# Kernel optimization log

Hardware: AMD Instinct MI355X
Metric: run time of the kernel (lower is better)

## Reference

```python
import jax, jax.numpy as jnp
import numpy as np

EMBED_DIM = 512
NUM_HEADS = 8
GLOBAL_MIX = 0.5


def setup_inputs() -> dict:
    key = jax.random.key(0)
    ks = jax.random.split(key, 7)
    B, L, E = 8, 1024, EMBED_DIM
    s = 1.0 / np.sqrt(E)
    x = jax.random.normal(ks[0], (B, L, E), dtype=jnp.float32)
    mask = jax.random.randint(ks[1], (B, L), 0, 2) > 0  # True = valid token
    Wq = jax.random.normal(ks[2], (E, E), dtype=jnp.float32) * s
    Wk = jax.random.normal(ks[3], (E, E), dtype=jnp.float32) * s
    Wv = jax.random.normal(ks[4], (E, E), dtype=jnp.float32) * s
    Wo = jax.random.normal(ks[5], (E, E), dtype=jnp.float32) * s
    G = jax.random.normal(ks[6], (L, L), dtype=jnp.float32)
    return {"x": x, "mask": mask, "Wq": Wq, "Wk": Wk, "Wv": Wv, "Wo": Wo, "G": G}


def _tanh_mha(x, mask, Wq, Wk, Wv, Wo, G):
    B, L, E = x.shape
    H = NUM_HEADS
    D = E // H
    scale = 1.0 / np.sqrt(D)
    dt = x.dtype
    fmax = jnp.finfo(dt).max
    tiny = jnp.finfo(dt).tiny

    def split_heads(t):  # (B,L,E) -> (B,H,L,D)
        return t.reshape(B, L, H, D).transpose(0, 2, 1, 3)

    q = split_heads(x @ Wq.T)
    k = split_heads(x @ Wk.T)
    v = split_heads(x @ Wv.T)

    scores = jnp.tanh(jnp.einsum('bhqd,bhkd->bhqk', q, k) * scale)
    key_valid = mask[:, None, None, :]  # (B,1,1,L)
    scores = jnp.where(key_valid, scores, -jnp.inf)

    finite = jnp.isfinite(scores)
    finite_scores = jnp.where(finite, scores, -fmax)
    m = jnp.max(finite_scores, axis=(1, 2, 3), keepdims=True)  # per-sample amax over heads+q+k
    m = jnp.where(jnp.isfinite(m), m, jnp.zeros_like(m))
    exp_scores = jnp.where(finite, jnp.exp(scores - m), jnp.zeros_like(scores))

    mf = mask.astype(dt)
    exp_scores = exp_scores * mf[:, None, None, :] * mf[:, None, :, None]
    denom = jnp.maximum(exp_scores.sum(axis=(1, 2, 3), keepdims=True), tiny)
    weights = exp_scores / denom
    # dropout p=0 -> identity; renorm pass kept for faithfulness
    renorm = jnp.maximum(weights.sum(axis=(1, 2, 3), keepdims=True), tiny)
    weights = weights / renorm

    # learnable global attention: softmax rows, clamp, mask, normalize over (q,k)
    activated = jnp.maximum(jax.nn.softmax(G, axis=-1), 0.0)  # (L,L)
    gscores = activated[None] * mf[:, None, :] * mf[:, :, None]  # (B,L,L)
    gsums = jnp.maximum(gscores.sum(axis=(1, 2), keepdims=True), tiny)
    gnorm = (gscores / gsums)[:, None]  # (B,1,L,L)
    weights = (1.0 - GLOBAL_MIX) * weights + GLOBAL_MIX * gnorm

    attended = jnp.einsum('bhqk,bhkd->bhqd', weights, v)
    attended = attended * mf[:, None, :, None]
    attended = attended.transpose(0, 2, 1, 3).reshape(B, L, E)
    return attended @ Wo.T


def reference(x, mask, Wq, Wk, Wv, Wo, G):
    return _tanh_mha(x, mask, Wq, Wk, Wv, Wo, G)
```

## Files before the change

### kernel.cpp

```cpp
#include <hip/hip_runtime.h>
#include <math.h>

#define B_ 8
#define L_ 1024
#define E_ 512
#define H_ 8
#define D_ 64
#define QSZ (B_*H_*L_*D_)
#define BLE ((size_t)B_*L_*E_)
#define TINYF 1.175494350822287508e-38f
#define SWK(r) ((((r) ^ ((r) >> 3))) & 7)

typedef unsigned short u16;
typedef __attribute__((ext_vector_type(8))) short bfrag;
typedef __attribute__((ext_vector_type(4))) float ffrag;
typedef __attribute__((ext_vector_type(16))) float ffrag16;
typedef __attribute__((ext_vector_type(4))) short vshort4;

#if __has_builtin(__builtin_amdgcn_exp2f)
#define EXP2F(x) __builtin_amdgcn_exp2f(x)
#else
#define EXP2F(x) __expf((x) * 0.6931471805599453f)
#endif
#if __has_builtin(__builtin_amdgcn_rcpf)
#define RCPF(x) __builtin_amdgcn_rcpf(x)
#else
#define RCPF(x) (1.0f / (x))
#endif

__device__ __forceinline__ u16 f2b(float f) {
  unsigned u = __float_as_uint(f);
  u += 0x7fffu + ((u >> 16) & 1u);
  return (u16)(u >> 16);
}
__device__ __forceinline__ unsigned pk2(float a, float b) {
  unsigned ua = __float_as_uint(a); ua += 0x7fffu + ((ua >> 16) & 1u);
  unsigned ub = __float_as_uint(b); ub += 0x7fffu + ((ub >> 16) & 1u);
  return (ua >> 16) | (ub & 0xffff0000u);
}
__device__ __forceinline__ float blo(unsigned u) { return __uint_as_float(u << 16); }
__device__ __forceinline__ float bhi(unsigned u) { return __uint_as_float(u & 0xffff0000u); }

__device__ __forceinline__ bfrag cvt8v(const float* __restrict__ src) {
  float4 a = *(const float4*)src;
  float4 b = *(const float4*)(src + 4);
  bfrag r;
  r[0]=(short)f2b(a.x); r[1]=(short)f2b(a.y); r[2]=(short)f2b(a.z); r[3]=(short)f2b(a.w);
  r[4]=(short)f2b(b.x); r[5]=(short)f2b(b.y); r[6]=(short)f2b(b.z); r[7]=(short)f2b(b.w);
  return r;
}

__device__ __forceinline__ void gll16(const void* g, void* l) {
  __builtin_amdgcn_global_load_lds(
      (const __attribute__((address_space(1))) void*)g,
      (__attribute__((address_space(3))) void*)l, 16, 0, 0);
}

__global__ __launch_bounds__(256) void prep_softmax_k(
    const float* __restrict__ x, const float* __restrict__ Wq,
    const float* __restrict__ Wk, const float* __restrict__ Wv,
    const float* __restrict__ Wo, const float* __restrict__ G,
    const int* __restrict__ mask,
    u16* __restrict__ xb, u16* __restrict__ Wb, u16* __restrict__ actb,
    float* __restrict__ R) {
  const int bid = blockIdx.x, t = threadIdx.x;
  __shared__ float sred[8];
  __shared__ float rred[4][8];
  if (bid < 2048) {
    size_t c = (size_t)bid * 256 + t;
    *(bfrag*)&xb[c * 8] = cvt8v(x + c * 8);
    return;
  }
  if (bid < 2560) {
    const int c2 = bid - 2048;
    const float* src = (c2 < 128) ? Wq : (c2 < 256) ? Wk : (c2 < 384) ? Wv : Wo;
    const size_t base = (size_t)(c2 >> 7) * 262144;
    const size_t cc = (size_t)(c2 & 127) * 256 + t;
    *(bfrag*)&Wb[base + cc * 8] = cvt8v(src + cc * 8);
    return;
  }
  const int q = bid - 2560;
  const int w = t >> 6, lane = t & 63;
  float4 g4 = ((const float4*)(G + (size_t)q * 1024))[t];
  float m = fmaxf(fmaxf(g4.x, g4.y), fmaxf(g4.z, g4.w));
#pragma unroll
  for (int off = 32; off > 0; off >>= 1) m = fmaxf(m, __shfl_down(m, off));
  if (lane == 0) sred[w] = m;
  __syncthreads();
  m = fmaxf(fmaxf(sred[0], sred[1]), fmaxf(sred[2], sred[3]));
  float e0 = __expf(g4.x - m), e1 = __expf(g4.y - m);
  float e2 = __expf(g4.z - m), e3 = __expf(g4.w - m);
  float s = e0 + e1 + e2 + e3;
#pragma unroll
  for (int off = 32; off > 0; off >>= 1) s += __shfl_down(s, off);
  if (lane == 0) sred[4 + w] = s;
  __syncthreads();
  const float inv = 1.0f / (sred[4] + sred[5] + sred[6] + sred[7]);
  const unsigned p0 = pk2(e0 * inv, e1 * inv);
  const unsigned p1 = pk2(e2 * inv, e3 * inv);
  *(uint2*)&actb[(size_t)q * 1024 + t * 4] = make_uint2(p0, p1);
  const float r0 = blo(p0), r1 = bhi(p0);
  const float r2 = blo(p1), r3 = bhi(p1);
  float rd[8];
#pragma unroll
  for (int b = 0; b < 8; ++b) {
    const int* mkp = mask + b * 1024 + t * 4;
    rd[b] = (mkp[0] ? r0 : 0.f) + (mkp[1] ? r1 : 0.f) +
            (mkp[2] ? r2 : 0.f) + (mkp[3] ? r3 : 0.f);
#pragma unroll
    for (int off = 32; off > 0; off >>= 1) rd[b] += __shfl_down(rd[b], off);
  }
  if (lane == 0)
#pragma unroll
    for (int b = 0; b < 8; ++b) rred[w][b] = rd[b];
  __syncthreads();
  if (t < 8) R[q * 8 + t] = rred[0][t] + rred[1][t] + rred[2][t] + rred[3][t];
}

__global__ __launch_bounds__(256) void proj_k(
    const u16* __restrict__ xb, const u16* __restrict__ Wb,
    const int* __restrict__ mask, const float* __restrict__ R,
    float* __restrict__ sums,
    u16* __restrict__ Qb, u16* __restrict__ Kb, u16* __restrict__ Vtb) {
  const int m0 = blockIdx.x * 128;
  const int n0 = blockIdx.y * 64;
  __shared__ u16 As[128 * 64];
  __shared__ u16 Bs[64 * 64];
  __shared__ float rr[4][8];
  const int t = threadIdx.x, w = t >> 6, lane = t & 63;
  const int l15 = lane & 15, quad = lane >> 4;
  const int x7 = l15 & 7;

  if (blockIdx.x == 0 && blockIdx.y == 0) {
    float a8[8] = {0,0,0,0,0,0,0,0};
    for (int q = t; q < 1024; q += 256)
#pragma unroll
      for (int b = 0; b < 8; ++b)
        if (mask[b * 1024 + q]) a8[b] += R[q * 8 + b];
#pragma unroll
    for (int b = 0; b < 8; ++b) {
#pragma unroll
      for (int off = 32; off > 0; off >>= 1) a8[b] += __shfl_down(a8[b], off);
    }
    if (lane == 0)
#pragma unroll
      for (int b = 0; b < 8; ++b) rr[w][b] = a8[b];
    __syncthreads();
    if (t < 8) {
      sums[t] = 0.0f;
      sums[8 + t] = rr[0][t] + rr[1][t] + rr[2][t] + rr[3][t];
    }
  }

  const ffrag fz = {0.f, 0.f, 0.f, 0.f};
  ffrag acc[2][4];
#pragma unroll
  for (int am = 0; am < 2; ++am)
#pragma unroll
    for (int bn = 0; bn < 4; ++bn) acc[am][bn] = fz;

  for (int kk = 0; kk < 512; kk += 64) {
    __syncthreads();
#pragma unroll
    for (int j = 0; j < 4; ++j) {
      const int c = w * 256 + j * 64 + lane;
      const int row = c >> 3, ck = (c & 7) ^ (row & 7);
      gll16(xb + (size_t)(m0 + row) * 512 + kk + ck * 8,
            &As[(size_t)(w * 256 + j * 64) * 8]);
    }
#pragma unroll
    for (int j = 0; j < 2; ++j) {
      const int c = w * 128 + j * 64 + lane;
      const int row = c >> 3, ck = (c & 7) ^ (row & 7);
      gll16(Wb + (size_t)(n0 + row) * 512 + kk + ck * 8,
            &Bs[(size_t)(w * 128 + j * 64) * 8]);
    }
    __syncthreads();
#pragma unroll
    for (int s = 0; s < 2; ++s) {
      const int co = ((quad + 4 * s) ^ x7) << 3;
      bfrag a0 = *(const bfrag*)&As[(w * 32 + l15) * 64 + co];
      bfrag a1 = *(const bfrag*)&As[(w * 32 + 16 + l15) * 64 + co];
#pragma unroll
      for (int bn = 0; bn < 4; ++bn) {
        bfrag bb = *(const bfrag*)&Bs[(bn * 16 + l15) * 64 + co];
        acc[0][bn] = __builtin_amdgcn_mfma_f32_16x16x32_bf16(a0, bb, acc[0][bn], 0, 0, 0);
        acc[1][bn] = __builtin_amdgcn_mfma_f32_16x16x32_bf16(a1, bb, acc[1][bn], 0, 0, 0);
      }
    }
  }
  const int z = n0 >> 9;
  const int c0 = n0 & 511;
#pragma unroll
  for (int am = 0; am < 2; ++am) {
    const int mbase = m0 + w * 32 + am * 16 + quad * 4;
    const int b = mbase >> 10, l0 = mbase & 1023;
#pragma unroll
    for (int bn = 0; bn < 4; ++bn) {
      const int nc = c0 + bn * 16 + l15;
      const int h = nc >> 6, d = nc & 63;
      if (z == 0) {
        u16* dst = Qb + ((size_t)(b * 8 + h) * 1024 + l0) * 64 + d;
#pragma unroll
        for (int r = 0; r < 4; ++r) dst[(size_t)r * 64] = f2b(acc[am][bn][r]);
      } else if (z == 1) {
        u16* dst = Kb + ((size_t)(b * 8 + h) * 1024 + l0) * 64 + d;
#pragma unroll
        for (int r = 0; r < 4; ++r) dst[(size_t)r * 64] = f2b(acc[am][bn][r]);
      } else {
        vshort4 vs;
#pragma unroll
        for (int r = 0; r < 4; ++r)
          vs[r] = (short)(mask[b * 1024 + l0 + r] ? f2b(acc[am][bn][r]) : (u16)0);
        *(vshort4*)(Vtb + ((size_t)(b * 8 + h) * 64 + d) * 1024 + l0) = vs;
      }
    }
  }
}

__global__ __launch_bounds__(256) void attn_k(
    const u16* __restrict__ Qb, const u16* __restrict__ Kb,
    const u16* __restrict__ Vtb, const u16* __restrict__ actb,
    const int* __restrict__ mask,
    u16* __restrict__ AEb, u16* __restrict__ AGb, float* __restrict__ denom) {
  const int qt = blockIdx.x;
  const int bh = blockIdx.y;
  const int b = bh >> 3, h = bh & 7;
  __shared__ __align__(16) u16 Ks[64 * 64];
  __shared__ __align__(16) u16 Vs[64 * 64];
  __shared__ __align__(16) u16 Acts[64 * 64];
  __shared__ __align__(16) u16 Es[64 * 64];
  __shared__ __align__(16) u16 Ms[1024];
  __shared__ float red4[4];
  const int t = threadIdx.x, w = t >> 6, lane = t & 63;
  const int l31 = lane & 31, hi = lane >> 5;
  const int qsb = w >> 1, msb = w & 1;
  const int qpb = w & 1, dpb = w >> 1;

  const u16* Kg = Kb + (size_t)bh * 65536;
  const u16* Vg = Vtb + (size_t)bh * 65536;
  const u16* Ag = actb + (size_t)(qt * 64) * 1024;

  const u16* Qrow = Qb + ((size_t)bh * 1024 + qt * 64 + qsb * 32 + l31) * 64;
  bfrag qf[4];
#pragma unroll
  for (int ko = 0; ko < 4; ++ko) qf[ko] = *(const bfrag*)(Qrow + ko * 16 + hi * 8);

  {
    int4 mi = *(const int4*)(mask + b * 1024 + t * 4);
    vshort4 mv;
    mv[0] = mi.x ? (short)0x3F80 : (short)0; mv[1] = mi.y ? (short)0x3F80 : (short)0;
    mv[2] = mi.z ? (short)0x3F80 : (short)0; mv[3] = mi.w ? (short)0x3F80 : (short)0;
    *(vshort4*)&Ms[t * 4] = mv;
  }

  auto stageK = [&](int kt) {
#pragma unroll
    for (int j = 0; j < 2; ++j) {
      const int c = w * 128 + j * 64 + lane;
      const int row = c >> 3, ck = (c & 7) ^ SWK(row);
      gll16(Kg + (size_t)(kt * 64 + row) * 64 + ck * 8,
            &Ks[(size_t)(w * 128 + j * 64) * 8]);
    }
  };
  auto stageV = [&](int kt) {
#pragma unroll
    for (int j = 0; j < 2; ++j) {
      const int c = w * 128 + j * 64 + lane;
      const int row = c >> 3, ck = (c & 7) ^ SWK(row);
      gll16(Vg + (size_t)row * 1024 + kt * 64 + ck * 8,
            &Vs[(size_t)(w * 128 + j * 64) * 8]);
    }
  };
  auto stageA = [&](int kt) {
#pragma unroll
    for (int j = 0; j < 2; ++j) {
      const int c = w * 128 + j * 64 + lane;
      const int row = c >> 3, ck = (c & 7) ^ SWK(row);
      gll16(Ag + (size_t)row * 1024 + kt * 64 + ck * 8,
            &Acts[(size_t)(w * 128 + j * 64) * 8]);
    }
  };

  stageK(0); stageV(0); stageA(0);
  __syncthreads();

  ffrag16 accE, accG, dacc;
#pragma unroll
  for (int i = 0; i < 16; ++i) { accE[i] = 0.f; accG[i] = 0.f; dacc[i] = 0.f; }

  for (int kt = 0; kt < 16; ++kt) {
    ffrag16 st;
#pragma unroll
    for (int i = 0; i < 16; ++i) st[i] = 0.f;
    const int krow = msb * 32 + l31;
    const int kk7 = SWK(krow);
#pragma unroll
    for (int ko = 0; ko < 4; ++ko) {
      bfrag ak = *(const bfrag*)&Ks[krow * 64 + (((ko * 2 + hi) ^ kk7) << 3)];
      st = __builtin_amdgcn_mfma_f32_32x32x16_bf16(ak, qf[ko], st, 0, 0, 0);
    }
    const int qrow = qsb * 32 + l31;
    const int qk7 = SWK(qrow);
#pragma unroll
    for (int g = 0; g < 4; ++g) {
      float ee[4];
#pragma unroll
      for (int r = 0; r < 4; ++r) {
        const float tt = EXP2F(st[4 * g + r] * 0.360673760222f);
        ee[r] = EXP2F(RCPF(tt + 1.0f) * -2.88539008178f);
      }
      const int k0 = msb * 32 + g * 8 + hi * 4;
      *(uint2*)&Es[qrow * 64 + (((k0 >> 3) ^ qk7) << 3) + (k0 & 7)] =
          make_uint2(pk2(ee[0], ee[1]), pk2(ee[2], ee[3]));
    }
    __syncthreads();
    if (kt < 15) stageK(kt + 1);

    const int erow = qpb * 32 + l31;
    const int ek7 = SWK(erow);
    const int vrow = dpb * 32 + l31;
    const int vk7 = SWK(vrow);
#pragma unroll
    for (int ko = 0; ko < 4; ++ko) {
      const int co = ko * 2 + hi;
      bfrag ea = *(const bfrag*)&Es[erow * 64 + ((co ^ ek7) << 3)];
      bfrag aa = *(const bfrag*)&Acts[erow * 64 + ((co ^ ek7) << 3)];
      bfrag bv = *(const bfrag*)&Vs[vrow * 64 + ((co ^ vk7) << 3)];
      accE = __builtin_amdgcn_mfma_f32_32x32x16_bf16(ea, bv, accE, 0, 0, 0);
      accG = __builtin_amdgcn_mfma_f32_32x32x16_bf16(aa, bv, accG, 0, 0, 0);
      if (dpb == 0) {
        bfrag bm = *(const bfrag*)&Ms[kt * 64 + ko * 16 + hi * 8];
        dacc = __builtin_amdgcn_mfma_f32_32x32x16_bf16(ea, bm, dacc, 0, 0, 0);
      }
    }
    __syncthreads();
    if (kt < 15) { stageV(kt + 1); stageA(kt + 1); }
  }

  const size_t obase = ((size_t)(b * 1024 + qt * 64 + qpb * 32)) * 512
                       + h * 64 + dpb * 32 + l31;
#pragma unroll
  for (int r = 0; r < 16; ++r) {
    const int qloc = (r & 3) + 8 * (r >> 2) + 4 * hi;
    AEb[obase + (size_t)qloc * 512] = f2b(accE[r]);
    AGb[obase + (size_t)qloc * 512] = f2b(accG[r]);
  }
  float dsumv = 0.0f;
  if (l31 == 0 && dpb == 0) {
    const int qb0 = b * 1024 + qt * 64 + qpb * 32 + 4 * hi;
#pragma unroll
    for (int r = 0; r < 16; ++r) {
      const int q = qb0 + (r & 3) + 8 * (r >> 2);
      dsumv += mask[q] ? dacc[r] : 0.0f;
    }
    red4[qpb * 2 + hi] = dsumv;
  }
  __syncthreads();
  if (t == 0) atomicAdd(denom + b, red4[0] + red4[1] + red4[2] + red4[3]);
}

__global__ __launch_bounds__(256) void o_proj_k(
    const u16* __restrict__ AEb, const u16* __restrict__ AGb,
    const int* __restrict__ mask, const float* __restrict__ sums,
    const u16* __restrict__ Wb, float* __restrict__ out) {
  const int m0 = blockIdx.x * 128;
  const int n0 = blockIdx.y * 64;
  const int b = m0 >> 10;
  const float c1 = 0.5f / fmaxf(sums[b], TINYF);
  const float c2 = 0.5f / fmaxf(sums[8 + b], TINYF);
  __shared__ __align__(16) u16 As[128 * 64];
  __shared__ __align__(16) u16 Bs[64 * 64];
  const int t = threadIdx.x, w = t >> 6, lane = t & 63;
  const int l15 = lane & 15, quad = lane >> 4;
  const int x7 = l15 & 7;
  int rowi[4]; float c1r[4], c2r[4];
#pragma unroll
  for (int i = 0; i < 4; ++i) {
    const int c = t + i * 256;
    rowi[i] = c >> 3;
    const int mq = mask[b * 1024 + ((m0 + rowi[i]) & 1023)];
    c1r[i] = mq ? c1 : 0.0f;
    c2r[i] = mq ? c2 : 0.0f;
  }
  const ffrag fz = {0.f, 0.f, 0.f, 0.f};
  ffrag acc[2][4];
#pragma unroll
  for (int am = 0; am < 2; ++am)
#pragma unroll
    for (int bn = 0; bn < 4; ++bn) acc[am][bn] = fz;

  for (int kk = 0; kk < 512; kk += 64) {
    __syncthreads();
#pragma unroll
    for (int i = 0; i < 4; ++i) {
      const int c = t + i * 256;
      const int row = rowi[i], ck = c & 7;
      const size_t gofs = (size_t)(m0 + row) * 512 + kk + ck * 8;
      uint4 ua = *(const uint4*)(AEb + gofs);
      uint4 ug = *(const uint4*)(AGb + gofs);
      const float a1 = c1r[i], a2 = c2r[i];
      uint4 res;
      res.x = pk2(a1 * blo(ua.x) + a2 * blo(ug.x), a1 * bhi(ua.x) + a2 * bhi(ug.x));
      res.y = pk2(a1 * blo(ua.y) + a2 * blo(ug.y), a1 * bhi(ua.y) + a2 * bhi(ug.y));
      res.z = pk2(a1 * blo(ua.z) + a2 * blo(ug.z), a1 * bhi(ua.z) + a2 * bhi(ug.z));
      res.w = pk2(a1 * blo(ua.w) + a2 * blo(ug.w), a1 * bhi(ua.w) + a2 * bhi(ug.w));
      *(uint4*)&As[row * 64 + ((ck ^ (row & 7)) << 3)] = res;
    }
#pragma unroll
    for (int j = 0; j < 2; ++j) {
      const int c = w * 128 + j * 64 + lane;
      const int row = c >> 3, ck = (c & 7) ^ (row & 7);
      gll16(Wb + (size_t)(1536 + n0 + row) * 512 + kk + ck * 8,
            &Bs[(size_t)(w * 128 + j * 64) * 8]);
    }
    __syncthreads();
#pragma unroll
    for (int s = 0; s < 2; ++s) {
      const int co = ((quad + 4 * s) ^ x7) << 3;
      bfrag a0 = *(const bfrag*)&As[(w * 32 + l15) * 64 + co];
      bfrag a1 = *(const bfrag*)&As[(w * 32 + 16 + l15) * 64 + co];
#pragma unroll
      for (int bn = 0; bn < 4; ++bn) {
        bfrag bb = *(const bfrag*)&Bs[(bn * 16 + l15) * 64 + co];
        acc[0][bn] = __builtin_amdgcn_mfma_f32_16x16x32_bf16(a0, bb, acc[0][bn], 0, 0, 0);
        acc[1][bn] = __builtin_amdgcn_mfma_f32_16x16x32_bf16(a1, bb, acc[1][bn], 0, 0, 0);
      }
    }
  }
#pragma unroll
  for (int am = 0; am < 2; ++am) {
    const int mbase = m0 + w * 32 + am * 16 + quad * 4;
#pragma unroll
    for (int bn = 0; bn < 4; ++bn) {
      const int n = n0 + bn * 16 + l15;
#pragma unroll
      for (int r = 0; r < 4; ++r)
        out[(size_t)(mbase + r) * 512 + n] = acc[am][bn][r];
    }
  }
}

extern "C" void kernel_launch(void* const* d_in, const int* in_sizes, int n_in,
                              void* d_out, int out_size, void* d_ws, size_t ws_size,
                              hipStream_t stream) {
  const float* x  = (const float*)d_in[0];
  const int* mask = (const int*)d_in[1];
  const float* Wq = (const float*)d_in[2];
  const float* Wk = (const float*)d_in[3];
  const float* Wv = (const float*)d_in[4];
  const float* Wo = (const float*)d_in[5];
  const float* G  = (const float*)d_in[6];
  float* out = (float*)d_out;

  u16* xb   = (u16*)d_ws;
  u16* Wb   = xb + (size_t)8192 * 512;
  u16* Qb   = Wb + (size_t)2048 * 512;
  u16* Kb   = Qb + QSZ;
  u16* Vtb  = Kb + QSZ;
  u16* actb = Vtb + QSZ;
  u16* AEb  = actb + (size_t)1024 * 1024;
  u16* AGb  = AEb + BLE;
  float* R  = (float*)(AGb + BLE);
  float* SUMS = R + 8192;

  prep_softmax_k<<<3584, 256, 0, stream>>>(x, Wq, Wk, Wv, Wo, G, mask, xb, Wb, actb, R);
  proj_k<<<dim3(64, 24), 256, 0, stream>>>(xb, Wb, mask, R, SUMS, Qb, Kb, Vtb);
  attn_k<<<dim3(16, 64), 256, 0, stream>>>(Qb, Kb, Vtb, actb, mask, AEb, AGb, SUMS);
  o_proj_k<<<dim3(64, 8), 256, 0, stream>>>(AEb, AGb, mask, SUMS, Wb, out);
}
```

Before: 195.9 us.

## Double-buffer attention tiles and keep probabilities in registers via lane shuffles

The attention kernel now double-buffers the K, V and activation tiles and prefetches the next tile at the start of each iteration, so only one barrier per key tile remains instead of two. The exp-of-tanh weights are repacked into MFMA A-operand fragments with cross-half-wave shuffles instead of being written to and re-read from a shared-memory E tile. Work is split across waves by key half rather than by output-column half, so each wave keeps two accumulators per output and the key halves are summed through shared memory at the end. This uses more LDS and registers, which may lower occupancy, and adds a final cross-wave reduction.

```diff
diff --git a/kernel.cpp b/kernel.cpp
--- a/kernel.cpp
+++ b/kernel.cpp
@@ -226,22 +226,20 @@
   const int qt = blockIdx.x;
   const int bh = blockIdx.y;
   const int b = bh >> 3, h = bh & 7;
-  __shared__ __align__(16) u16 Ks[64 * 64];
-  __shared__ __align__(16) u16 Vs[64 * 64];
-  __shared__ __align__(16) u16 Acts[64 * 64];
-  __shared__ __align__(16) u16 Es[64 * 64];
+  __shared__ __align__(16) u16 Ks[2][64 * 64];
+  __shared__ __align__(16) u16 Vs[2][64 * 64];
+  __shared__ __align__(16) u16 Acts[2][64 * 64];
   __shared__ __align__(16) u16 Ms[1024];
-  __shared__ float red4[4];
+  __shared__ float red8[8];
   const int t = threadIdx.x, w = t >> 6, lane = t & 63;
   const int l31 = lane & 31, hi = lane >> 5;
-  const int qsb = w >> 1, msb = w & 1;
-  const int qpb = w & 1, dpb = w >> 1;
+  const int qb2 = w >> 1, kb = w & 1;
 
   const u16* Kg = Kb + (size_t)bh * 65536;
   const u16* Vg = Vtb + (size_t)bh * 65536;
   const u16* Ag = actb + (size_t)(qt * 64) * 1024;
 
-  const u16* Qrow = Qb + ((size_t)bh * 1024 + qt * 64 + qsb * 32 + l31) * 64;
+  const u16* Qrow = Qb + ((size_t)bh * 1024 + qt * 64 + qb2 * 32 + l31) * 64;
   bfrag qf[4];
 #pragma unroll
   for (int ko = 0; ko < 4; ++ko) qf[ko] = *(const bfrag*)(Qrow + ko * 16 + hi * 8);
@@ -254,110 +252,134 @@
     *(vshort4*)&Ms[t * 4] = mv;
   }
 
-  auto stageK = [&](int kt) {
+  auto stageAll = [&](int p, int kt) {
 #pragma unroll
     for (int j = 0; j < 2; ++j) {
       const int c = w * 128 + j * 64 + lane;
       const int row = c >> 3, ck = (c & 7) ^ SWK(row);
       gll16(Kg + (size_t)(kt * 64 + row) * 64 + ck * 8,
-            &Ks[(size_t)(w * 128 + j * 64) * 8]);
+            &Ks[p][(size_t)(w * 128 + j * 64) * 8]);
+      gll16(Vg + (size_t)row * 1024 + kt * 64 + ck * 8,
+            &Vs[p][(size_t)(w * 128 + j * 64) * 8]);
+      gll16(Ag + (size_t)row * 1024 + kt * 64 + ck * 8,
+            &Acts[p][(size_t)(w * 128 + j * 64) * 8]);
     }
   };
-  auto stageV = [&](int kt) {
-#pragma unroll
-    for (int j = 0; j < 2; ++j) {
-      const int c = w * 128 + j * 64 + lane;
-      const int row = c >> 3, ck = (c & 7) ^ SWK(row);
-      gll16(Vg + (size_t)row * 1024 + kt * 64 + ck * 8,
-            &Vs[(size_t)(w * 128 + j * 64) * 8]);
-    }
-  };
-  auto stageA = [&](int kt) {
-#pragma unroll
-    for (int j = 0; j < 2; ++j) {
-      const int c = w * 128 + j * 64 + lane;
-      const int row = c >> 3, ck = (c & 7) ^ SWK(row);
-      gll16(Ag + (size_t)row * 1024 + kt * 64 + ck * 8,
-            &Acts[(size_t)(w * 128 + j * 64) * 8]);
-    }
-  };
-
-  stageK(0); stageV(0); stageA(0);
+
+  stageAll(0, 0);
   __syncthreads();
 
-  ffrag16 accE, accG, dacc;
-#pragma unroll
-  for (int i = 0; i < 16; ++i) { accE[i] = 0.f; accG[i] = 0.f; dacc[i] = 0.f; }
+  ffrag16 accE[2], accG[2], dacc;
+#pragma unroll
+  for (int i = 0; i < 16; ++i) {
+    accE[0][i] = 0.f; accE[1][i] = 0.f; accG[0][i] = 0.f; accG[1][i] = 0.f;
+    dacc[i] = 0.f;
+  }
+
+  const int krow = kb * 32 + l31;
+  const int kk7 = SWK(krow);
+  const int arow = qb2 * 32 + l31;
+  const int ak7 = SWK(arow);
 
   for (int kt = 0; kt < 16; ++kt) {
+    const int p = kt & 1;
+    if (kt < 15) stageAll(1 - p, kt + 1);
+
     ffrag16 st;
 #pragma unroll
     for (int i = 0; i < 16; ++i) st[i] = 0.f;
-    const int krow = msb * 32 + l31;
-    const int kk7 = SWK(krow);
 #pragma unroll
     for (int ko = 0; ko < 4; ++ko) {
-      bfrag ak = *(const bfrag*)&Ks[krow * 64 + (((ko * 2 + hi) ^ kk7) << 3)];
+      bfrag ak = *(const bfrag*)&Ks[p][krow * 64 + (((ko * 2 + hi) ^ kk7) << 3)];
       st = __builtin_amdgcn_mfma_f32_32x32x16_bf16(ak, qf[ko], st, 0, 0, 0);
     }
-    const int qrow = qsb * 32 + l31;
-    const int qk7 = SWK(qrow);
-#pragma unroll
-    for (int g = 0; g < 4; ++g) {
-      float ee[4];
-#pragma unroll
-      for (int r = 0; r < 4; ++r) {
-        const float tt = EXP2F(st[4 * g + r] * 0.360673760222f);
-        ee[r] = EXP2F(RCPF(tt + 1.0f) * -2.88539008178f);
-      }
-      const int k0 = msb * 32 + g * 8 + hi * 4;
-      *(uint2*)&Es[qrow * 64 + (((k0 >> 3) ^ qk7) << 3) + (k0 & 7)] =
-          make_uint2(pk2(ee[0], ee[1]), pk2(ee[2], ee[3]));
-    }
-    __syncthreads();
-    if (kt < 15) stageK(kt + 1);
-
-    const int erow = qpb * 32 + l31;
-    const int ek7 = SWK(erow);
-    const int vrow = dpb * 32 + l31;
-    const int vk7 = SWK(vrow);
-#pragma unroll
-    for (int ko = 0; ko < 4; ++ko) {
-      const int co = ko * 2 + hi;
-      bfrag ea = *(const bfrag*)&Es[erow * 64 + ((co ^ ek7) << 3)];
-      bfrag aa = *(const bfrag*)&Acts[erow * 64 + ((co ^ ek7) << 3)];
-      bfrag bv = *(const bfrag*)&Vs[vrow * 64 + ((co ^ vk7) << 3)];
-      accE = __builtin_amdgcn_mfma_f32_32x32x16_bf16(ea, bv, accE, 0, 0, 0);
-      accG = __builtin_amdgcn_mfma_f32_32x32x16_bf16(aa, bv, accG, 0, 0, 0);
-      if (dpb == 0) {
-        bfrag bm = *(const bfrag*)&Ms[kt * 64 + ko * 16 + hi * 8];
-        dacc = __builtin_amdgcn_mfma_f32_32x32x16_bf16(ea, bm, dacc, 0, 0, 0);
-      }
-    }
-    __syncthreads();
-    if (kt < 15) { stageV(kt + 1); stageA(kt + 1); }
-  }
-
-  const size_t obase = ((size_t)(b * 1024 + qt * 64 + qpb * 32)) * 512
-                       + h * 64 + dpb * 32 + l31;
-#pragma unroll
-  for (int r = 0; r < 16; ++r) {
-    const int qloc = (r & 3) + 8 * (r >> 2) + 4 * hi;
-    AEb[obase + (size_t)qloc * 512] = f2b(accE[r]);
-    AGb[obase + (size_t)qloc * 512] = f2b(accG[r]);
+
+    unsigned P[8];
+#pragma unroll
+    for (int j = 0; j < 8; ++j) {
+      const float t0 = EXP2F(st[2 * j] * 0.360673760222f);
+      const float e0 = EXP2F(RCPF(t0 + 1.0f) * -2.88539008178f);
+      const float t1 = EXP2F(st[2 * j + 1] * 0.360673760222f);
+      const float e1 = EXP2F(RCPF(t1 + 1.0f) * -2.88539008178f);
+      P[j] = pk2(e0, e1);
+    }
+    bfrag ef[2];
+#pragma unroll
+    for (int g = 0; g < 2; ++g) {
+      const unsigned q0 = P[4 * g + 0], q1 = P[4 * g + 1];
+      const unsigned q2 = P[4 * g + 2], q3 = P[4 * g + 3];
+      const unsigned r0 = (unsigned)__shfl_xor((int)q0, 32);
+      const unsigned r1 = (unsigned)__shfl_xor((int)q1, 32);
+      const unsigned r2 = (unsigned)__shfl_xor((int)q2, 32);
+      const unsigned r3 = (unsigned)__shfl_xor((int)q3, 32);
+      union { uint4 u; bfrag f; } cv;
+      cv.u.x = hi ? r2 : q0;
+      cv.u.y = hi ? r3 : q1;
+      cv.u.z = hi ? q2 : r0;
+      cv.u.w = hi ? q3 : r1;
+      ef[g] = cv.f;
+    }
+
+#pragma unroll
+    for (int ko = 0; ko < 2; ++ko) {
+      bfrag bm = *(const bfrag*)&Ms[kt * 64 + kb * 32 + ko * 16 + hi * 8];
+      dacc = __builtin_amdgcn_mfma_f32_32x32x16_bf16(ef[ko], bm, dacc, 0, 0, 0);
+    }
+
+#pragma unroll
+    for (int ko = 0; ko < 2; ++ko) {
+      const int co = kb * 4 + ko * 2 + hi;
+      bfrag aa = *(const bfrag*)&Acts[p][arow * 64 + ((co ^ ak7) << 3)];
+#pragma unroll
+      for (int db = 0; db < 2; ++db) {
+        const int vrow = db * 32 + l31;
+        bfrag bv = *(const bfrag*)&Vs[p][vrow * 64 + ((co ^ SWK(vrow)) << 3)];
+        accE[db] = __builtin_amdgcn_mfma_f32_32x32x16_bf16(ef[ko], bv, accE[db], 0, 0, 0);
+        accG[db] = __builtin_amdgcn_mfma_f32_32x32x16_bf16(aa, bv, accG[db], 0, 0, 0);
+      }
+    }
+    __syncthreads();
+  }
+
+  float* redE = (float*)Ks;
+  float* redG = (float*)Vs;
+  if (kb == 1) {
+#pragma unroll
+    for (int db = 0; db < 2; ++db)
+#pragma unroll
+      for (int r = 0; r < 16; ++r) {
+        redE[(qb2 * 2 + db) * 1024 + r * 64 + lane] = accE[db][r];
+        redG[(qb2 * 2 + db) * 1024 + r * 64 + lane] = accG[db][r];
+      }
   }
   float dsumv = 0.0f;
-  if (l31 == 0 && dpb == 0) {
-    const int qb0 = b * 1024 + qt * 64 + qpb * 32 + 4 * hi;
+  if (l31 == 0) {
+    const int qb0 = b * 1024 + qt * 64 + qb2 * 32 + 4 * hi;
 #pragma unroll
     for (int r = 0; r < 16; ++r) {
       const int q = qb0 + (r & 3) + 8 * (r >> 2);
       dsumv += mask[q] ? dacc[r] : 0.0f;
     }
-    red4[qpb * 2 + hi] = dsumv;
+    red8[w * 2 + hi] = dsumv;
   }
   __syncthreads();
-  if (t == 0) atomicAdd(denom + b, red4[0] + red4[1] + red4[2] + red4[3]);
+  if (kb == 0) {
+    const size_t obase = ((size_t)(b * 1024 + qt * 64 + qb2 * 32)) * 512
+                         + h * 64 + l31;
+#pragma unroll
+    for (int db = 0; db < 2; ++db)
+#pragma unroll
+      for (int r = 0; r < 16; ++r) {
+        const float vE = accE[db][r] + redE[(qb2 * 2 + db) * 1024 + r * 64 + lane];
+        const float vG = accG[db][r] + redG[(qb2 * 2 + db) * 1024 + r * 64 + lane];
+        const int qloc = (r & 3) + 8 * (r >> 2) + 4 * hi;
+        AEb[obase + db * 32 + (size_t)qloc * 512] = f2b(vE);
+        AGb[obase + db * 32 + (size_t)qloc * 512] = f2b(vG);
+      }
+  }
+  if (t == 0)
+    atomicAdd(denom + b, red8[0] + red8[1] + red8[2] + red8[3] +
+                         red8[4] + red8[5] + red8[6] + red8[7]);
 }
 
 __global__ __launch_bounds__(256) void o_proj_k(
```

Result: slower. 199.8 us (+2.0%).
